# Kernel optimization log

Hardware: AMD Instinct MI355X
Metric: run time of the kernel (lower is better)

The kernel has to match this reference:

```python
import jax, jax.numpy as jnp
import numpy as np

B, M, D = 8, 1024, 1024
H = 16
HD = D // H  # 64
F = 4096

def layer_norm(x, gamma, beta, eps=1e-5):
    mu = jnp.mean(x, axis=-1, keepdims=True)
    var = jnp.var(x, axis=-1, keepdims=True)
    return (x - mu) * jax.lax.rsqrt(var + eps) * gamma + beta

def setup_inputs() -> dict:
    key = jax.random.key(0)
    ks = jax.random.split(key, 16)
    s = 0.02
    return {
        "h": jax.random.normal(ks[0], (B, M, D), jnp.float32),
        "h_all": jax.random.normal(ks[1], (B, M, D), jnp.float32),
        "Wq": jax.random.normal(ks[2], (D, D), jnp.float32) * s,
        "Wk": jax.random.normal(ks[3], (D, D), jnp.float32) * s,
        "Wv": jax.random.normal(ks[4], (D, D), jnp.float32) * s,
        "Wo": jax.random.normal(ks[5], (D, D), jnp.float32) * s,
        "W1": jax.random.normal(ks[6], (D, F), jnp.float32) * s,
        "b1": jnp.zeros((F,), jnp.float32),
        "W2": jax.random.normal(ks[7], (F, D), jnp.float32) * s,
        "b2": jnp.zeros((D,), jnp.float32),
        "g1": jnp.ones((D,), jnp.float32),
        "be1": jnp.zeros((D,), jnp.float32),
        "g2": jnp.ones((D,), jnp.float32),
        "be2": jnp.zeros((D,), jnp.float32),
    }

def reference(h, h_all, Wq, Wk, Wv, Wo, W1, b1, W2, b2, g1, be1, g2, be2):
    Bx, Mx, Dx = h.shape
    # projections (no bias, per nn.Linear(bias=False))
    q = (h @ Wq).reshape(Bx, Mx, H, HD)        # [B,M,H,hd]
    k = (h_all @ Wk).reshape(Bx, -1, H, HD)    # [B,N,H,hd]
    v = (h_all @ Wv).reshape(Bx, -1, H, HD)
    # attention: scale by sqrt(head_dim) as in SeqAttention(hidden_size=head_dim)
    scores = jnp.einsum('bqhd,bkhd->bhqk', q, k) / jnp.sqrt(jnp.float32(HD))
    attn = jax.nn.softmax(scores, axis=-1)
    ctx = jnp.einsum('bhqk,bkhd->bqhd', attn, v).reshape(Bx, Mx, Dx)
    attn_out = ctx @ Wo
    # post-norm residual 1
    h1 = layer_norm(h + attn_out, g1, be1)
    # FFN
    ff = jax.nn.relu(h1 @ W1 + b1) @ W2 + b2
    # post-norm residual 2
    out = layer_norm(h1 + ff, g2, be2)
    return out
```

## Files before the change

### kernel.cpp

```cpp
#include <hip/hip_runtime.h>
#include <hip/hip_bf16.h>

#define ROWS 8192
#define DD   1024
#define HH   16
#define HD   64
#define FF   4096

typedef __attribute__((ext_vector_type(4))) float f32x4;
typedef __attribute__((ext_vector_type(8))) __bf16 bf16x8;

static __device__ __forceinline__ unsigned short f2bf(float f) {
  unsigned u = __float_as_uint(f);
  u += 0x7fffu + ((u >> 16) & 1u);
  return (unsigned short)(u >> 16);
}

static __device__ __forceinline__ f32x4 mfma16(bf16x8 a, bf16x8 b, f32x4 c) {
  return __builtin_amdgcn_mfma_f32_16x16x32_bf16(a, b, c, 0, 0, 0);
}

#define GLOAD16(gp, lp) __builtin_amdgcn_global_load_lds( \
    (__attribute__((address_space(1))) void*)(gp), \
    (__attribute__((address_space(3))) void*)(lp), 16, 0, 0)

__global__ __launch_bounds__(256) void cast_bf16_k(
    const float* __restrict__ in, unsigned short* __restrict__ out, int n4) {
  int i = blockIdx.x * 256 + threadIdx.x;
  if (i >= n4) return;
  float4 v = ((const float4*)in)[i];
  ushort4 o;
  o.x = f2bf(v.x); o.y = f2bf(v.y); o.z = f2bf(v.z); o.w = f2bf(v.w);
  ((ushort4*)out)[i] = o;
}

__global__ __launch_bounds__(256) void transpose_cast_k(
    const float* __restrict__ in, unsigned short* __restrict__ out, int R, int C) {
  __shared__ float tile[32][33];
  int bx = blockIdx.x * 32;
  int by = blockIdx.y * 32;
  int tx = threadIdx.x, ty = threadIdx.y;
  #pragma unroll
  for (int i = 0; i < 32; i += 8)
    tile[ty + i][tx] = in[(size_t)(by + ty + i) * C + bx + tx];
  __syncthreads();
  #pragma unroll
  for (int i = 0; i < 32; i += 8)
    out[(size_t)(bx + ty + i) * R + by + tx] = f2bf(tile[tx][ty + i]);
}

template <int BM, int MODE, int KS = 1>
__global__ __launch_bounds__(512, 2) void gemm256(
    const unsigned short* __restrict__ A, const unsigned short* __restrict__ BT,
    const float* __restrict__ bias, void* __restrict__ Cout, void* __restrict__ Cout2,
    int Ni, int Ki, int nbx) {
  constexpr int LA = BM / 64;
  constexpr int MR = BM / 32;
  __shared__ unsigned short As[2][BM * 64];
  __shared__ unsigned short Bs[2][256 * 64];

  const int tid  = threadIdx.x;
  const int lane = tid & 63;
  const int wid  = tid >> 6;
  const int wm   = wid >> 2;
  const int wn   = wid & 3;
  const int lr   = lane & 15;
  const int kq   = lane >> 4;
  const int axor = (lr & 7) << 4;

  const int nwg = gridDim.x;
  const int cpx = nwg >> 3;
  const int wg  = (int)blockIdx.x;
  const int swz = (wg & 7) * cpx + (wg >> 3);
  const int perk = nwg / KS;
  const int kh   = swz / perk;
  const int swzr = swz % perk;
  const int bx = swzr % nbx, by = swzr / nbx;
  const int brow = by * BM, bcol = bx * 256;
  const int Kc   = Ki / KS;
  const int kbase = kh * Kc;

  const int srow = wid * 8 + (lane >> 3);
  const int scol = ((lane & 7) * 8) ^ ((srow & 7) << 3);
  size_t offA[LA], offB[4];
  #pragma unroll
  for (int L = 0; L < LA; ++L)
    offA[L] = (size_t)(brow + L * 64 + srow) * Ki + kbase + scol;
  #pragma unroll
  for (int L = 0; L < 4; ++L)
    offB[L] = (size_t)(bcol + L * 64 + srow) * Ki + kbase + scol;

  auto stage = [&](int t, int d) {
    #pragma unroll
    for (int L = 0; L < LA; ++L)
      GLOAD16(A + offA[L] + t * 64, (char*)As[d] + L * 8192 + wid * 1024);
    #pragma unroll
    for (int L = 0; L < 4; ++L)
      GLOAD16(BT + offB[L] + t * 64, (char*)Bs[d] + L * 8192 + wid * 1024);
  };

  f32x4 acc[MR][4] = {};
  const int NT = Kc >> 6;

  stage(0, 0);
  stage(1, 1);

  #pragma unroll 1
  for (int t = 0; t < NT; ++t) {
    const int d = t & 1;
    if constexpr (BM == 256) asm volatile("s_waitcnt vmcnt(8)" ::: "memory");
    else                     asm volatile("s_waitcnt vmcnt(6)" ::: "memory");
    __builtin_amdgcn_s_barrier();
    __builtin_amdgcn_sched_barrier(0);

    const unsigned short* as = As[d];
    const unsigned short* bs = Bs[d];
    #pragma unroll
    for (int kk = 0; kk < 2; ++kk) {
      bf16x8 af[MR], bfv[4];
      #pragma unroll
      for (int m = 0; m < MR; ++m)
        af[m] = *(const bf16x8*)((const char*)as +
            (wm * (BM / 2) + m * 16 + lr) * 128 + ((kk * 64 + kq * 16) ^ axor));
      #pragma unroll
      for (int n = 0; n < 4; ++n)
        bfv[n] = *(const bf16x8*)((const char*)bs +
            (wn * 64 + n * 16 + lr) * 128 + ((kk * 64 + kq * 16) ^ axor));
      #pragma unroll
      for (int m = 0; m < MR; ++m)
        #pragma unroll
        for (int n = 0; n < 4; ++n)
          acc[m][n] = mfma16(af[m], bfv[n], acc[m][n]);
    }

    asm volatile("s_waitcnt lgkmcnt(0)" ::: "memory");
    __builtin_amdgcn_s_barrier();
    __builtin_amdgcn_sched_barrier(0);
    const int ts = (t + 2 < NT) ? t + 2 : NT - 1;
    stage(ts, d);
  }

  #pragma unroll
  for (int m = 0; m < MR; ++m) {
    #pragma unroll
    for (int n = 0; n < 4; ++n) {
      const int r0 = brow + wm * (BM / 2) + m * 16 + kq * 4;
      const int c  = bcol + wn * 64 + n * 16 + lr;
      if constexpr (MODE == 4) {
        if (c < 1024) {
          #pragma unroll
          for (int e = 0; e < 4; ++e)
            ((unsigned short*)Cout)[(size_t)(r0 + e) * 1024 + c] = f2bf(acc[m][n][e]);
        } else {
          const int cc = c - 1024;
          const int bq = r0 >> 10;
          const int tok = r0 & 1023;
          ushort4 pk;
          pk.x = f2bf(acc[m][n][0]); pk.y = f2bf(acc[m][n][1]);
          pk.z = f2bf(acc[m][n][2]); pk.w = f2bf(acc[m][n][3]);
          *(ushort4*)((unsigned short*)Cout2 + ((size_t)bq * 1024 + cc) * 1024 + tok) = pk;
        }
      } else if constexpr (MODE == 5) {
        float* o = (kh == 0) ? (float*)Cout : (float*)Cout2;
        const float bv = (kh == 0) ? bias[c] : 0.0f;
        #pragma unroll
        for (int e = 0; e < 4; ++e)
          o[(size_t)(r0 + e) * Ni + c] = acc[m][n][e] + bv;
      } else {
        const float bv = (MODE == 2 || MODE == 3) ? bias[c] : 0.0f;
        #pragma unroll
        for (int e = 0; e < 4; ++e) {
          float v = acc[m][n][e] + bv;
          if (MODE == 2) v = fmaxf(v, 0.0f);
          if (MODE == 0 || MODE == 2)
            ((unsigned short*)Cout)[(size_t)(r0 + e) * Ni + c] = f2bf(v);
          else
            ((float*)Cout)[(size_t)(r0 + e) * Ni + c] = v;
        }
      }
    }
  }
}

__global__ __launch_bounds__(512, 6) void attn_k(
    const unsigned short* __restrict__ q, const unsigned short* __restrict__ k,
    const unsigned short* __restrict__ vT, unsigned short* __restrict__ ctx) {
  __shared__ unsigned short Ks[2][64 * 64];
  __shared__ unsigned short Vt[2][64 * 64];
  __shared__ unsigned short Ps[8][16 * 64];
  const int tid = threadIdx.x;
  const int lane = tid & 63;
  const int wid = tid >> 6;
  const int bh = blockIdx.y;
  const int b = bh >> 4, h = bh & 15;
  const int qrow0 = blockIdx.x * 128 + wid * 16;
  const size_t tokbase = (size_t)b * 1024;
  const int lr = lane & 15, kq = lane >> 4;

  const int srow = tid >> 3;
  const int scol = ((tid & 7) * 8) ^ ((srow & 7) << 3);
  const unsigned short* kg = k + (tokbase + srow) * 1024 + h * 64 + scol;
  const unsigned short* vg = vT + ((size_t)(b * 16 + h) * 64 + srow) * 1024 + scol;
  const int ldst = tid * 16;

  auto stage = [&](int kt, int d) {
    GLOAD16(kg + (size_t)kt * 64 * 1024, (char*)Ks[d] + ldst);
    GLOAD16(vg + kt * 64, (char*)Vt[d] + ldst);
  };

  bf16x8 aq[2];
  {
    const unsigned short* qp = q + (tokbase + qrow0 + lr) * DD + h * 64 + kq * 8;
    aq[0] = *(const bf16x8*)qp;
    aq[1] = *(const bf16x8*)(qp + 32);
  }

  float l_part[4] = {0.f, 0.f, 0.f, 0.f};
  f32x4 acc[4] = {};
  const float C = 0.125f * 1.4426950408889634f;

  stage(0, 0);
  stage(1, 1);

  #pragma unroll 2
  for (int kt = 0; kt < 16; ++kt) {
    const int d = kt & 1;
    asm volatile("s_waitcnt vmcnt(2)" ::: "memory");
    __builtin_amdgcn_s_barrier();
    __builtin_amdgcn_sched_barrier(0);

    f32x4 sv[4] = {};
    #pragma unroll
    for (int jb = 0; jb < 4; ++jb)
      #pragma unroll
      for (int ks = 0; ks < 2; ++ks) {
        int row = jb * 16 + lr;
        bf16x8 bk = *(const bf16x8*)((const char*)Ks[d] +
            row * 128 + ((ks * 64 + kq * 16) ^ ((row & 7) << 4)));
        sv[jb] = mfma16(aq[ks], bk, sv[jb]);
      }

    #pragma unroll
    for (int jb = 0; jb < 4; ++jb)
      #pragma unroll
      for (int j = 0; j < 4; ++j) {
        float p = exp2f(sv[jb][j] * C);
        sv[jb][j] = p;
        l_part[j] += p;
      }

    #pragma unroll
    for (int jb = 0; jb < 4; ++jb)
      #pragma unroll
      for (int j = 0; j < 4; ++j) {
        int row = kq * 4 + j;
        *(unsigned short*)((char*)Ps[wid] +
            ((row * 128 + (jb * 16 + lr) * 2) ^ ((row & 7) << 4))) = f2bf(sv[jb][j]);
      }

    #pragma unroll
    for (int ks = 0; ks < 2; ++ks) {
      bf16x8 ap = *(const bf16x8*)((const char*)Ps[wid] +
          lr * 128 + ((ks * 64 + kq * 16) ^ ((lr & 7) << 4)));
      #pragma unroll
      for (int db = 0; db < 4; ++db) {
        int dd = db * 16 + lr;
        bf16x8 bv = *(const bf16x8*)((const char*)Vt[d] +
            dd * 128 + ((ks * 64 + kq * 16) ^ ((dd & 7) << 4)));
        acc[db] = mfma16(ap, bv, acc[db]);
      }
    }

    asm volatile("s_waitcnt lgkmcnt(0)" ::: "memory");
    __builtin_amdgcn_s_barrier();
    __builtin_amdgcn_sched_barrier(0);
    const int ts = (kt + 2 < 16) ? kt + 2 : 15;
    stage(ts, d);
  }

  #pragma unroll
  for (int j = 0; j < 4; ++j) {
    float l = l_part[j];
    #pragma unroll
    for (int mk = 1; mk < 16; mk <<= 1) l += __shfl_xor(l, mk);
    float inv = 1.0f / l;
    int r = qrow0 + kq * 4 + j;
    #pragma unroll
    for (int db = 0; db < 4; ++db)
      ctx[(tokbase + r) * DD + h * 64 + db * 16 + lr] = f2bf(acc[db][j] * inv);
  }
}

template <int WB>
__global__ __launch_bounds__(256) void ln_add_k(
    const float* __restrict__ a, const float* __restrict__ b,
    const float* __restrict__ gamma, const float* __restrict__ beta,
    float* __restrict__ outf, unsigned short* __restrict__ outb) {
  int row = blockIdx.x;
  int tid = threadIdx.x;
  size_t base = (size_t)row * 1024 + tid * 4;
  float4 va = *(const float4*)(a + base);
  float4 vb = *(const float4*)(b + base);
  float x[4] = {va.x + vb.x, va.y + vb.y, va.z + vb.z, va.w + vb.w};
  float s = x[0] + x[1] + x[2] + x[3];
  float sq = x[0] * x[0] + x[1] * x[1] + x[2] * x[2] + x[3] * x[3];
  #pragma unroll
  for (int mk = 1; mk < 64; mk <<= 1) {
    s += __shfl_xor(s, mk);
    sq += __shfl_xor(sq, mk);
  }
  __shared__ float red[8];
  int wid = tid >> 6, lane = tid & 63;
  if (lane == 0) { red[wid] = s; red[4 + wid] = sq; }
  __syncthreads();
  s = red[0] + red[1] + red[2] + red[3];
  sq = red[4] + red[5] + red[6] + red[7];
  float mu = s * (1.0f / 1024.0f);
  float var = sq * (1.0f / 1024.0f) - mu * mu;
  float rs = rsqrtf(var + 1e-5f);
  float4 g = *(const float4*)(gamma + tid * 4);
  float4 be = *(const float4*)(beta + tid * 4);
  float y[4];
  y[0] = (x[0] - mu) * rs * g.x + be.x;
  y[1] = (x[1] - mu) * rs * g.y + be.y;
  y[2] = (x[2] - mu) * rs * g.z + be.z;
  y[3] = (x[3] - mu) * rs * g.w + be.w;
  float4 o; o.x = y[0]; o.y = y[1]; o.z = y[2]; o.w = y[3];
  *(float4*)(outf + base) = o;
  if (WB) {
    ushort4 ob;
    ob.x = f2bf(y[0]); ob.y = f2bf(y[1]); ob.z = f2bf(y[2]); ob.w = f2bf(y[3]);
    *(ushort4*)(outb + base) = ob;
  }
}

__global__ __launch_bounds__(256) void ln3_k(
    const float* __restrict__ a, const float* __restrict__ b,
    const float* __restrict__ c,
    const float* __restrict__ gamma, const float* __restrict__ beta,
    float* __restrict__ outf) {
  int row = blockIdx.x;
  int tid = threadIdx.x;
  size_t base = (size_t)row * 1024 + tid * 4;
  float4 va = *(const float4*)(a + base);
  float4 vb = *(const float4*)(b + base);
  float4 vc = *(const float4*)(c + base);
  float x[4] = {va.x + vb.x + vc.x, va.y + vb.y + vc.y,
                va.z + vb.z + vc.z, va.w + vb.w + vc.w};
  float s = x[0] + x[1] + x[2] + x[3];
  float sq = x[0] * x[0] + x[1] * x[1] + x[2] * x[2] + x[3] * x[3];
  #pragma unroll
  for (int mk = 1; mk < 64; mk <<= 1) {
    s += __shfl_xor(s, mk);
    sq += __shfl_xor(sq, mk);
  }
  __shared__ float red[8];
  int wid = tid >> 6, lane = tid & 63;
  if (lane == 0) { red[wid] = s; red[4 + wid] = sq; }
  __syncthreads();
  s = red[0] + red[1] + red[2] + red[3];
  sq = red[4] + red[5] + red[6] + red[7];
  float mu = s * (1.0f / 1024.0f);
  float var = sq * (1.0f / 1024.0f) - mu * mu;
  float rs = rsqrtf(var + 1e-5f);
  float4 g = *(const float4*)(gamma + tid * 4);
  float4 be = *(const float4*)(beta + tid * 4);
  float4 o;
  o.x = (x[0] - mu) * rs * g.x + be.x;
  o.y = (x[1] - mu) * rs * g.y + be.y;
  o.z = (x[2] - mu) * rs * g.z + be.z;
  o.w = (x[3] - mu) * rs * g.w + be.w;
  *(float4*)(outf + base) = o;
}

extern "C" void kernel_launch(void* const* d_in, const int* in_sizes, int n_in,
                              void* d_out, int out_size, void* d_ws, size_t ws_size,
                              hipStream_t stream) {
  const float* h    = (const float*)d_in[0];
  const float* hall = (const float*)d_in[1];
  const float* Wq   = (const float*)d_in[2];
  const float* Wk   = (const float*)d_in[3];
  const float* Wv   = (const float*)d_in[4];
  const float* Wo   = (const float*)d_in[5];
  const float* W1   = (const float*)d_in[6];
  const float* b1   = (const float*)d_in[7];
  const float* W2   = (const float*)d_in[8];
  const float* b2   = (const float*)d_in[9];
  const float* g1   = (const float*)d_in[10];
  const float* be1  = (const float*)d_in[11];
  const float* g2   = (const float*)d_in[12];
  const float* be2  = (const float*)d_in[13];

  char* ws = (char*)d_ws;
  size_t off = 0;
  auto alloc = [&](size_t n) { size_t o = off; off += (n + 255) & ~(size_t)255; return o; };
  const size_t hb_o   = alloc((size_t)ROWS * DD * 2);
  const size_t hab_o  = alloc((size_t)ROWS * DD * 2);
  const size_t wqt_o  = alloc((size_t)DD * DD * 2);
  const size_t wkvt_o = alloc((size_t)DD * DD * 4);
  const size_t wot_o  = alloc((size_t)DD * DD * 2);
  const size_t w1t_o  = alloc((size_t)DD * FF * 2);
  const size_t w2t_o  = alloc((size_t)FF * DD * 2);
  const size_t qb_o   = alloc((size_t)ROWS * DD * 2);
  const size_t kb_o   = alloc((size_t)ROWS * DD * 2);
  const size_t vt_o   = alloc((size_t)ROWS * DD * 2);
  const size_t cx_o   = alloc((size_t)ROWS * DD * 2);
  const size_t h1_o   = alloc((size_t)ROWS * DD * 4);
  const size_t h1b_o  = alloc((size_t)ROWS * DD * 2);

  unsigned short* hb   = (unsigned short*)(ws + hb_o);
  unsigned short* hab  = (unsigned short*)(ws + hab_o);
  unsigned short* wqt  = (unsigned short*)(ws + wqt_o);
  unsigned short* wkvt = (unsigned short*)(ws + wkvt_o);
  unsigned short* wot  = (unsigned short*)(ws + wot_o);
  unsigned short* w1t  = (unsigned short*)(ws + w1t_o);
  unsigned short* w2t  = (unsigned short*)(ws + w2t_o);
  unsigned short* qb   = (unsigned short*)(ws + qb_o);
  unsigned short* kb   = (unsigned short*)(ws + kb_o);
  unsigned short* vTb  = (unsigned short*)(ws + vt_o);
  unsigned short* cxb  = (unsigned short*)(ws + cx_o);
  float*          h1   = (float*)(ws + h1_o);
  unsigned short* h1b  = (unsigned short*)(ws + h1b_o);
  float*          attn_out = (float*)(ws + hb_o);
  float*          ff2p1    = (float*)(ws + hb_o);
  unsigned short* ff1      = (unsigned short*)(ws + qb_o);
  float*          outf     = (float*)d_out;

  cast_bf16_k<<<ROWS * DD / 1024, 256, 0, stream>>>(h, hb, ROWS * DD / 4);
  cast_bf16_k<<<ROWS * DD / 1024, 256, 0, stream>>>(hall, hab, ROWS * DD / 4);
  dim3 tb(32, 8);
  transpose_cast_k<<<dim3(32, 32), tb, 0, stream>>>(Wq, wqt, DD, DD);
  transpose_cast_k<<<dim3(32, 32), tb, 0, stream>>>(Wk, wkvt, DD, DD);
  transpose_cast_k<<<dim3(32, 32), tb, 0, stream>>>(Wv, wkvt + (size_t)DD * DD, DD, DD);
  transpose_cast_k<<<dim3(32, 32), tb, 0, stream>>>(Wo, wot, DD, DD);
  transpose_cast_k<<<dim3(128, 32), tb, 0, stream>>>(W1, w1t, DD, FF);
  transpose_cast_k<<<dim3(32, 128), tb, 0, stream>>>(W2, w2t, FF, DD);

  gemm256<128, 0><<<dim3(256), 512, 0, stream>>>(hb,  wqt,  nullptr, qb, nullptr, DD,   DD, 4);
  gemm256<256, 4><<<dim3(256), 512, 0, stream>>>(hab, wkvt, nullptr, kb, vTb,    2048, DD, 8);

  attn_k<<<dim3(8, 128), 512, 0, stream>>>(qb, kb, vTb, cxb);

  gemm256<128, 1><<<dim3(256), 512, 0, stream>>>(cxb, wot, nullptr, attn_out, nullptr, DD, DD, 4);
  ln_add_k<1><<<ROWS, 256, 0, stream>>>(h, attn_out, g1, be1, h1, h1b);

  gemm256<256, 2>   <<<dim3(512), 512, 0, stream>>>(h1b, w1t, b1, ff1, nullptr, FF, DD, 16);
  gemm256<256, 5, 2><<<dim3(256), 512, 0, stream>>>(ff1, w2t, b2, outf, ff2p1, DD, FF, 4);

  ln3_k<<<ROWS, 256, 0, stream>>>(h1, outf, ff2p1, g2, be2, outf);
}
```

Measured before the change: 391.2 us.

## Software-pipeline LDS fragment loads with MFMA in BM=256 GEMM main loop

For the BM=256 GEMM variant, the inner loop is restructured to preload all B fragments and double-buffer A fragments in groups of two rows. The loads for the next group are issued while MFMAs on the current group run. s_setprio raises wave priority around the MFMA bursts, and a barrier per sub-step keeps the waves in lockstep. The intent is to hide LDS read latency behind matrix work. The cost is more registers, extra barriers per tile, and possible occupancy loss.

```diff
diff --git a/kernel.cpp b/kernel.cpp
--- a/kernel.cpp
+++ b/kernel.cpp
@@ -105,39 +105,92 @@
   stage(0, 0);
   stage(1, 1);
 
-  #pragma unroll 1
-  for (int t = 0; t < NT; ++t) {
-    const int d = t & 1;
-    if constexpr (BM == 256) asm volatile("s_waitcnt vmcnt(8)" ::: "memory");
-    else                     asm volatile("s_waitcnt vmcnt(6)" ::: "memory");
-    __builtin_amdgcn_s_barrier();
-    __builtin_amdgcn_sched_barrier(0);
-
-    const unsigned short* as = As[d];
-    const unsigned short* bs = Bs[d];
-    #pragma unroll
-    for (int kk = 0; kk < 2; ++kk) {
-      bf16x8 af[MR], bfv[4];
-      #pragma unroll
-      for (int m = 0; m < MR; ++m)
-        af[m] = *(const bf16x8*)((const char*)as +
-            (wm * (BM / 2) + m * 16 + lr) * 128 + ((kk * 64 + kq * 16) ^ axor));
+  if constexpr (BM == 256) {
+    #pragma unroll 1
+    for (int t = 0; t < NT; ++t) {
+      const int d = t & 1;
+      asm volatile("s_waitcnt vmcnt(8)" ::: "memory");
+      __builtin_amdgcn_s_barrier();
+      __builtin_amdgcn_sched_barrier(0);
+      const unsigned short* as = As[d];
+      const unsigned short* bs = Bs[d];
+      bf16x8 bfv[4][2];
+      bf16x8 afp[2][2][2];
       #pragma unroll
       for (int n = 0; n < 4; ++n)
-        bfv[n] = *(const bf16x8*)((const char*)bs +
-            (wn * 64 + n * 16 + lr) * 128 + ((kk * 64 + kq * 16) ^ axor));
-      #pragma unroll
-      for (int m = 0; m < MR; ++m)
+        #pragma unroll
+        for (int ks = 0; ks < 2; ++ks)
+          bfv[n][ks] = *(const bf16x8*)((const char*)bs +
+              (wn * 64 + n * 16 + lr) * 128 + ((ks * 64 + kq * 16) ^ axor));
+      #pragma unroll
+      for (int mm = 0; mm < 2; ++mm)
+        #pragma unroll
+        for (int ks = 0; ks < 2; ++ks)
+          afp[0][mm][ks] = *(const bf16x8*)((const char*)as +
+              (wm * 128 + mm * 16 + lr) * 128 + ((ks * 64 + kq * 16) ^ axor));
+      #pragma unroll
+      for (int q = 0; q < 4; ++q) {
+        asm volatile("s_waitcnt lgkmcnt(0)" ::: "memory");
+        __builtin_amdgcn_sched_barrier(0);
+        __builtin_amdgcn_s_setprio(1);
+        #pragma unroll
+        for (int mm = 0; mm < 2; ++mm)
+          #pragma unroll
+          for (int n = 0; n < 4; ++n) {
+            acc[q * 2 + mm][n] = mfma16(afp[q & 1][mm][0], bfv[n][0], acc[q * 2 + mm][n]);
+            acc[q * 2 + mm][n] = mfma16(afp[q & 1][mm][1], bfv[n][1], acc[q * 2 + mm][n]);
+          }
+        __builtin_amdgcn_s_setprio(0);
+        __builtin_amdgcn_sched_barrier(0);
+        if (q < 3) {
+          #pragma unroll
+          for (int mm = 0; mm < 2; ++mm)
+            #pragma unroll
+            for (int ks = 0; ks < 2; ++ks)
+              afp[(q + 1) & 1][mm][ks] = *(const bf16x8*)((const char*)as +
+                  (wm * 128 + ((q + 1) * 2 + mm) * 16 + lr) * 128 +
+                  ((ks * 64 + kq * 16) ^ axor));
+        }
+        __builtin_amdgcn_s_barrier();
+      }
+      __builtin_amdgcn_sched_barrier(0);
+      const int ts = (t + 2 < NT) ? t + 2 : NT - 1;
+      stage(ts, d);
+    }
+  } else {
+    #pragma unroll 1
+    for (int t = 0; t < NT; ++t) {
+      const int d = t & 1;
+      asm volatile("s_waitcnt vmcnt(6)" ::: "memory");
+      __builtin_amdgcn_s_barrier();
+      __builtin_amdgcn_sched_barrier(0);
+
+      const unsigned short* as = As[d];
+      const unsigned short* bs = Bs[d];
+      #pragma unroll
+      for (int kk = 0; kk < 2; ++kk) {
+        bf16x8 af[MR], bfv[4];
+        #pragma unroll
+        for (int m = 0; m < MR; ++m)
+          af[m] = *(const bf16x8*)((const char*)as +
+              (wm * (BM / 2) + m * 16 + lr) * 128 + ((kk * 64 + kq * 16) ^ axor));
         #pragma unroll
         for (int n = 0; n < 4; ++n)
-          acc[m][n] = mfma16(af[m], bfv[n], acc[m][n]);
+          bfv[n] = *(const bf16x8*)((const char*)bs +
+              (wn * 64 + n * 16 + lr) * 128 + ((kk * 64 + kq * 16) ^ axor));
+        #pragma unroll
+        for (int m = 0; m < MR; ++m)
+          #pragma unroll
+          for (int n = 0; n < 4; ++n)
+            acc[m][n] = mfma16(af[m], bfv[n], acc[m][n]);
+      }
+
+      asm volatile("s_waitcnt lgkmcnt(0)" ::: "memory");
+      __builtin_amdgcn_s_barrier();
+      __builtin_amdgcn_sched_barrier(0);
+      const int ts = (t + 2 < NT) ? t + 2 : NT - 1;
+      stage(ts, d);
     }
-
-    asm volatile("s_waitcnt lgkmcnt(0)" ::: "memory");
-    __builtin_amdgcn_s_barrier();
-    __builtin_amdgcn_sched_barrier(0);
-    const int ts = (t + 2 < NT) ? t + 2 : NT - 1;
-    stage(ts, d);
   }
 
   #pragma unroll
```

Measured after the change: 401.1 us. 1.03x slower.

## Split BM=256 GEMM K-tile into half-stages with finer-grained LDS pipelining

Applied to the files above, without the earlier changes.

For the BM=256 GEMM variant, each 64-wide K tile is split into two 32-wide half stages, each with its own LDS buffer. Loads for the next half stage are issued right after the current fragments are read, which cuts one barrier per half step. The LDS layout changes to 64-byte rows with a new XOR swizzle, and s_setprio raises wave priority around the MFMA block. The aim is to overlap global-to-LDS loads with MFMA work more tightly and reduce barrier stalls. The trade-off is more barrier points and vmcnt bookkeeping, with a risk of bank conflicts or waitcnt mistakes in the new layout.

```diff
diff --git a/kernel.cpp b/kernel.cpp
--- a/kernel.cpp
+++ b/kernel.cpp
@@ -54,10 +54,7 @@
     const unsigned short* __restrict__ A, const unsigned short* __restrict__ BT,
     const float* __restrict__ bias, void* __restrict__ Cout, void* __restrict__ Cout2,
     int Ni, int Ki, int nbx) {
-  constexpr int LA = BM / 64;
   constexpr int MR = BM / 32;
-  __shared__ unsigned short As[2][BM * 64];
-  __shared__ unsigned short Bs[2][256 * 64];
 
   const int tid  = threadIdx.x;
   const int lane = tid & 63;
@@ -66,7 +63,6 @@
   const int wn   = wid & 3;
   const int lr   = lane & 15;
   const int kq   = lane >> 4;
-  const int axor = (lr & 7) << 4;
 
   const int nwg = gridDim.x;
   const int cpx = nwg >> 3;
@@ -80,64 +76,129 @@
   const int Kc   = Ki / KS;
   const int kbase = kh * Kc;
 
-  const int srow = wid * 8 + (lane >> 3);
-  const int scol = ((lane & 7) * 8) ^ ((srow & 7) << 3);
-  size_t offA[LA], offB[4];
-  #pragma unroll
-  for (int L = 0; L < LA; ++L)
-    offA[L] = (size_t)(brow + L * 64 + srow) * Ki + kbase + scol;
-  #pragma unroll
-  for (int L = 0; L < 4; ++L)
-    offB[L] = (size_t)(bcol + L * 64 + srow) * Ki + kbase + scol;
-
-  auto stage = [&](int t, int d) {
-    #pragma unroll
-    for (int L = 0; L < LA; ++L)
-      GLOAD16(A + offA[L] + t * 64, (char*)As[d] + L * 8192 + wid * 1024);
-    #pragma unroll
-    for (int L = 0; L < 4; ++L)
-      GLOAD16(BT + offB[L] + t * 64, (char*)Bs[d] + L * 8192 + wid * 1024);
-  };
-
   f32x4 acc[MR][4] = {};
   const int NT = Kc >> 6;
 
-  stage(0, 0);
-  stage(1, 1);
-
-  #pragma unroll 1
-  for (int t = 0; t < NT; ++t) {
-    const int d = t & 1;
-    if constexpr (BM == 256) asm volatile("s_waitcnt vmcnt(8)" ::: "memory");
-    else                     asm volatile("s_waitcnt vmcnt(6)" ::: "memory");
-    __builtin_amdgcn_s_barrier();
-    __builtin_amdgcn_sched_barrier(0);
-
-    const unsigned short* as = As[d];
-    const unsigned short* bs = Bs[d];
-    #pragma unroll
-    for (int kk = 0; kk < 2; ++kk) {
-      bf16x8 af[MR], bfv[4];
-      #pragma unroll
-      for (int m = 0; m < MR; ++m)
-        af[m] = *(const bf16x8*)((const char*)as +
-            (wm * (BM / 2) + m * 16 + lr) * 128 + ((kk * 64 + kq * 16) ^ axor));
-      #pragma unroll
-      for (int n = 0; n < 4; ++n)
-        bfv[n] = *(const bf16x8*)((const char*)bs +
-            (wn * 64 + n * 16 + lr) * 128 + ((kk * 64 + kq * 16) ^ axor));
-      #pragma unroll
-      for (int m = 0; m < MR; ++m)
+  if constexpr (BM == 256) {
+    __shared__ unsigned short As[2 * 2 * 256 * 32];
+    __shared__ unsigned short Bs[2 * 2 * 256 * 32];
+
+    const int srow0 = tid >> 2;
+    const int csw   = ((tid & 3) ^ ((tid >> 3) & 3)) * 8;
+    const size_t sA0 = (size_t)(brow + srow0) * Ki + kbase + csw;
+    const size_t sB0 = (size_t)(bcol + srow0) * Ki + kbase + csw;
+    const int coff = ((kq ^ ((lr >> 1) & 3)) << 4);
+
+    auto stageu = [&](int srcT, int db, int ks) {
+      const size_t so = (size_t)srcT * 64 + ks * 32;
+      char* la = (char*)As + (db * 2 + ks) * 16384 + wid * 1024;
+      char* lb = (char*)Bs + (db * 2 + ks) * 16384 + wid * 1024;
+      GLOAD16(A + sA0 + so, la);
+      GLOAD16(A + sA0 + so + (size_t)128 * Ki, la + 8192);
+      GLOAD16(BT + sB0 + so, lb);
+      GLOAD16(BT + sB0 + so + (size_t)128 * Ki, lb + 8192);
+    };
+
+    stageu(0, 0, 0);
+    stageu(0, 0, 1);
+    stageu(1, 1, 0);
+
+    #pragma unroll 1
+    for (int t = 0; t < NT; ++t) {
+      const int d = t & 1;
+      #pragma unroll
+      for (int p = 0; p < 2; ++p) {
+        asm volatile("s_waitcnt vmcnt(8)" ::: "memory");
+        __builtin_amdgcn_s_barrier();
+        __builtin_amdgcn_sched_barrier(0);
+        const char* ab = (const char*)As + (d * 2 + p) * 16384;
+        const char* bb = (const char*)Bs + (d * 2 + p) * 16384;
+        bf16x8 af[8], bfv[4];
+        #pragma unroll
+        for (int m = 0; m < 8; ++m)
+          af[m] = *(const bf16x8*)(ab + (wm * 128 + m * 16 + lr) * 64 + coff);
         #pragma unroll
         for (int n = 0; n < 4; ++n)
-          acc[m][n] = mfma16(af[m], bfv[n], acc[m][n]);
+          bfv[n] = *(const bf16x8*)(bb + (wn * 64 + n * 16 + lr) * 64 + coff);
+        if (p == 0) {
+          const int ts = (t + 1 < NT) ? t + 1 : NT - 1;
+          stageu(ts, (t + 1) & 1, 1);
+        } else {
+          const int ts = (t + 2 < NT) ? t + 2 : NT - 1;
+          stageu(ts, d, 0);
+        }
+        asm volatile("s_waitcnt lgkmcnt(0)" ::: "memory");
+        __builtin_amdgcn_sched_barrier(0);
+        __builtin_amdgcn_s_setprio(1);
+        #pragma unroll
+        for (int m = 0; m < 8; ++m)
+          #pragma unroll
+          for (int n = 0; n < 4; ++n)
+            acc[m][n] = mfma16(af[m], bfv[n], acc[m][n]);
+        __builtin_amdgcn_s_setprio(0);
+        __builtin_amdgcn_sched_barrier(0);
+      }
     }
-
-    asm volatile("s_waitcnt lgkmcnt(0)" ::: "memory");
-    __builtin_amdgcn_s_barrier();
-    __builtin_amdgcn_sched_barrier(0);
-    const int ts = (t + 2 < NT) ? t + 2 : NT - 1;
-    stage(ts, d);
+    asm volatile("s_waitcnt vmcnt(0)" ::: "memory");
+  } else {
+    __shared__ unsigned short As[2][BM * 64];
+    __shared__ unsigned short Bs[2][256 * 64];
+    const int axor = (lr & 7) << 4;
+    const int srow = wid * 8 + (lane >> 3);
+    const int scol = ((lane & 7) * 8) ^ ((srow & 7) << 3);
+    size_t offA[BM / 64], offB[4];
+    #pragma unroll
+    for (int L = 0; L < BM / 64; ++L)
+      offA[L] = (size_t)(brow + L * 64 + srow) * Ki + kbase + scol;
+    #pragma unroll
+    for (int L = 0; L < 4; ++L)
+      offB[L] = (size_t)(bcol + L * 64 + srow) * Ki + kbase + scol;
+
+    auto stage = [&](int t, int d) {
+      #pragma unroll
+      for (int L = 0; L < BM / 64; ++L)
+        GLOAD16(A + offA[L] + t * 64, (char*)As[d] + L * 8192 + wid * 1024);
+      #pragma unroll
+      for (int L = 0; L < 4; ++L)
+        GLOAD16(BT + offB[L] + t * 64, (char*)Bs[d] + L * 8192 + wid * 1024);
+    };
+
+    stage(0, 0);
+    stage(1, 1);
+
+    #pragma unroll 1
+    for (int t = 0; t < NT; ++t) {
+      const int d = t & 1;
+      asm volatile("s_waitcnt vmcnt(6)" ::: "memory");
+      __builtin_amdgcn_s_barrier();
+      __builtin_amdgcn_sched_barrier(0);
+
+      const unsigned short* as = As[d];
+      const unsigned short* bs = Bs[d];
+      #pragma unroll
+      for (int kk = 0; kk < 2; ++kk) {
+        bf16x8 af[MR], bfv[4];
+        #pragma unroll
+        for (int m = 0; m < MR; ++m)
+          af[m] = *(const bf16x8*)((const char*)as +
+              (wm * (BM / 2) + m * 16 + lr) * 128 + ((kk * 64 + kq * 16) ^ axor));
+        #pragma unroll
+        for (int n = 0; n < 4; ++n)
+          bfv[n] = *(const bf16x8*)((const char*)bs +
+              (wn * 64 + n * 16 + lr) * 128 + ((kk * 64 + kq * 16) ^ axor));
+        #pragma unroll
+        for (int m = 0; m < MR; ++m)
+          #pragma unroll
+          for (int n = 0; n < 4; ++n)
+            acc[m][n] = mfma16(af[m], bfv[n], acc[m][n]);
+      }
+
+      asm volatile("s_waitcnt lgkmcnt(0)" ::: "memory");
+      __builtin_amdgcn_s_barrier();
+      __builtin_amdgcn_sched_barrier(0);
+      const int ts = (t + 2 < NT) ? t + 2 : NT - 1;
+      stage(ts, d);
+    }
   }
 
   #pragma unroll
```

Result: no change. 396.6 us (+1.4%).
